# Performance work log

Measured on AMD Instinct MI355X. Metric: run time of the kernel, lower is better.

The kernel has to match this reference:

```python
import jax, jax.numpy as jnp
import numpy as np

B, S, D = 4, 2048, 1024
NH = 16
H2 = NH // 2
F = D // NH  # per-head hidden = 64
EXP = 4
DECAY_CONST = S // 512  # 4
EPS = 1e-5


def setup_inputs() -> dict:
    key = jax.random.key(0)
    ks = jax.random.split(key, 8)
    inp = {
        "x": jax.random.normal(ks[0], (B, S, D), dtype=jnp.float32),
        # token_norm / channel_norm params (LayerNorm init: ones/zeros)
        "g1": jnp.ones((D,), jnp.float32), "b1": jnp.zeros((D,), jnp.float32),
        "g2": jnp.ones((D,), jnp.float32), "b2": jnp.zeros((D,), jnp.float32),
        # per-head input projections [NH, D, F] and output projection
        "Wp": jax.random.normal(ks[1], (NH, D, F), jnp.float32) * 0.02,
        "bp": jnp.zeros((NH, F), jnp.float32),
        "Wo": jax.random.normal(ks[2], (D, D), jnp.float32) * 0.02,
        "bo": jnp.zeros((D,), jnp.float32),
        # ColRepeatCausalLinear: weight = 0.4, bias = 3 ; RowRepeat: -0.3, 0.2
        "w_col": jnp.full((H2, S), 0.4, jnp.float32),
        "b_col": jnp.full((H2, S), 3.0, jnp.float32),
        "w_row": jnp.full((H2, S), -0.3, jnp.float32),
        "b_row": jnp.full((H2, S), 0.2, jnp.float32),
        # decay_value params (ones, clipped to [0.9, 1] then ** (1/decay_constant))
        "dcol": jnp.ones((H2,), jnp.float32),
        "drow": jnp.ones((H2,), jnp.float32),
        # channel MLP
        "W1": jax.random.normal(ks[3], (D, EXP * D), jnp.float32) * 0.02,
        "c1": jnp.zeros((EXP * D,), jnp.float32),
        "W2": jax.random.normal(ks[4], (EXP * D, D), jnp.float32) * 0.02,
        "c2": jnp.zeros((D,), jnp.float32),
    }
    return inp


def _ln(x, g, b):
    m = jnp.mean(x, axis=-1, keepdims=True)
    v = jnp.mean(jnp.square(x - m), axis=-1, keepdims=True)
    return (x - m) * jax.lax.rsqrt(v + EPS) * g + b


def _forward(x, g1, b1, g2, b2, Wp, bp, Wo, bo, w_col, b_col, w_row, b_row,
             dcol, drow, W1, c1, W2, c2):
    decay_c = jnp.clip(dcol, 0.9, 1.0) ** (1.0 / DECAY_CONST)  # [H2]
    decay_r = jnp.clip(drow, 0.9, 1.0) ** (1.0 / DECAY_CONST)  # [H2]

    def step(carry, inp):
        cc, rc = carry                      # each [B, H2, F]
        xt, wc, bc, wr, br = inp            # xt [B, D]; wc/bc/wr/br [H2]
        # token mixing branch
        h = _ln(xt, g1, b1)
        proj = jnp.einsum('bd,hdf->bhf', h, Wp) + bp  # [B, NH, F]
        # Col heads: cache = proj + decay*cache ; out = w*cache + b
        cc = proj[:, :H2] + decay_c[None, :, None] * cc
        col_out = wc[None, :, None] * cc + bc[None, :, None]
        # Row heads: cache = w*proj + decay*cache ; out = cache + b
        rc = wr[None, :, None] * proj[:, H2:] + decay_r[None, :, None] * rc
        row_out = rc + br[None, :, None]
        mix = jnp.concatenate([col_out, row_out], axis=1).reshape(xt.shape[0], -1)
        y = xt + mix @ Wo + bo
        # channel MLP branch
        h2 = _ln(y, g2, b2)
        out = y + jax.nn.gelu(h2 @ W1 + c1) @ W2 + c2
        return (cc, rc), out

    init = (jnp.zeros((x.shape[0], H2, F), x.dtype),
            jnp.zeros((x.shape[0], H2, F), x.dtype))
    xs = (jnp.swapaxes(x, 0, 1), w_col.T, b_col.T, w_row.T, b_row.T)
    _, ys = jax.lax.scan(step, init, xs)    # ys [S, B, D]
    return jnp.swapaxes(ys, 0, 1)


def reference(x, g1, b1, g2, b2, Wp, bp, Wo, bo, w_col, b_col, w_row, b_row,
              dcol, drow, W1, c1, W2, c2):
    return _forward(x, g1, b1, g2, b2, Wp, bp, Wo, bo, w_col, b_col,
                    w_row, b_row, dcol, drow, W1, c1, W2, c2)
```

## Files before the change

### kernel.cpp

```cpp
#include <hip/hip_runtime.h>

typedef __attribute__((ext_vector_type(4))) float fx4;
typedef __attribute__((ext_vector_type(8))) short s16x8;
typedef __attribute__((ext_vector_type(2))) unsigned long long u64x2;

#define SEQ   2048
#define DM    1024
#define BSZ   4
#define ROWS  (BSZ*SEQ)
#define CHUNK 64
#define NCH   (SEQ/CHUNK)

__device__ __forceinline__ unsigned short f2bf(float f){
  unsigned u = __builtin_bit_cast(unsigned, f);
  u = u + 0x7FFFu + ((u >> 16) & 1u);
  return (unsigned short)(u >> 16);
}
__device__ __forceinline__ float bf2f(unsigned short u){
  return __builtin_bit_cast(float, ((unsigned)u) << 16);
}

__device__ __forceinline__ unsigned char f2fp8(float x){
  unsigned u = __builtin_bit_cast(unsigned, x);
  unsigned s = (u >> 24) & 0x80u;
  float ax = __builtin_fabsf(x);
  if (ax >= 448.f) return (unsigned char)(s | 0x7Eu);
  if (ax < 0.015625f){
    int m = (int)(ax * 512.f + 0.5f);
    return (unsigned char)(s | (unsigned)m);
  }
  unsigned b = __builtin_bit_cast(unsigned, ax);
  b += 0x0007FFFFu + ((b >> 20) & 1u);
  unsigned e = (b >> 23) - 127u + 7u;
  unsigned m = (b >> 20) & 7u;
  return (unsigned char)(s | (e << 3) | m);
}

__device__ __forceinline__ float gelu_f(float x){
  float u = 0.7978845608028654f * (x + 0.044715f * x*x*x);
  return x / (1.0f + __expf(-2.0f*u));
}

__device__ __forceinline__ void gload_lds16(const void* g, void* l){
  __builtin_amdgcn_global_load_lds(
      (__attribute__((address_space(1))) void*)g,
      (__attribute__((address_space(3))) void*)l, 16, 0, 0);
}

__device__ __forceinline__ fx4 mfma_fp8(unsigned long long a, unsigned long long b, fx4 c){
  return __builtin_amdgcn_mfma_f32_16x16x32_fp8_fp8((long)a, (long)b, c, 0, 0, 0);
}

__global__ __launch_bounds__(256) void transpose_k(const float* __restrict__ in,
    unsigned short* __restrict__ out, int R, int C, long long ibs, long long obs){
  __shared__ float tile[32][33];
  in  += (long long)blockIdx.z * ibs;
  out += (long long)blockIdx.z * obs;
  int c0 = blockIdx.x*32, r0 = blockIdx.y*32;
  int tx = threadIdx.x, ty = threadIdx.y;
  #pragma unroll
  for (int i=0;i<4;i++)
    tile[ty+8*i][tx] = in[(long long)(r0+ty+8*i)*C + c0+tx];
  __syncthreads();
  #pragma unroll
  for (int i=0;i<4;i++)
    out[(long long)(c0+ty+8*i)*R + r0+tx] = f2bf(tile[tx][ty+8*i]);
}

__global__ __launch_bounds__(256) void transpose_f8(const float* __restrict__ in,
    unsigned char* __restrict__ out, int R, int C){
  __shared__ float tile[32][33];
  int c0 = blockIdx.x*32, r0 = blockIdx.y*32;
  int tx = threadIdx.x, ty = threadIdx.y;
  #pragma unroll
  for (int i=0;i<4;i++)
    tile[ty+8*i][tx] = in[(long long)(r0+ty+8*i)*C + c0+tx];
  __syncthreads();
  #pragma unroll
  for (int i=0;i<4;i++)
    out[(long long)(c0+ty+8*i)*R + r0+tx] = f2fp8(tile[tx][ty+8*i] * 64.f);
}

__global__ __launch_bounds__(256) void ln_rows(const float* __restrict__ x,
    const float* __restrict__ g, const float* __restrict__ b,
    unsigned short* __restrict__ out){
  int row = blockIdx.x, t = threadIdx.x;
  const fx4* xr = (const fx4*)(x + (long long)row*DM);
  fx4 v = xr[t];
  float s  = v[0]+v[1]+v[2]+v[3];
  float s2 = v[0]*v[0]+v[1]*v[1]+v[2]*v[2]+v[3]*v[3];
  #pragma unroll
  for (int o=32;o;o>>=1){ s += __shfl_down(s,o); s2 += __shfl_down(s2,o); }
  __shared__ float red[8];
  int lane = t & 63, wid = t >> 6;
  if (lane==0){ red[wid]=s; red[4+wid]=s2; }
  __syncthreads();
  s  = red[0]+red[1]+red[2]+red[3];
  s2 = red[4]+red[5]+red[6]+red[7];
  float m  = s * (1.0f/DM);
  float rs = rsqrtf(s2*(1.0f/DM) - m*m + 1e-5f);
  const fx4 gv = ((const fx4*)g)[t], bv = ((const fx4*)b)[t];
  ushort4 pk;
  pk.x = f2bf((v[0]-m)*rs*gv[0] + bv[0]);
  pk.y = f2bf((v[1]-m)*rs*gv[1] + bv[1]);
  pk.z = f2bf((v[2]-m)*rs*gv[2] + bv[2]);
  pk.w = f2bf((v[3]-m)*rs*gv[3] + bv[3]);
  *(ushort4*)(out + (long long)row*DM + t*4) = pk;
}

__global__ __launch_bounds__(256) void ln_rows_f8(const float* __restrict__ x,
    const float* __restrict__ g, const float* __restrict__ b,
    unsigned char* __restrict__ out){
  int row = blockIdx.x, t = threadIdx.x;
  const fx4* xr = (const fx4*)(x + (long long)row*DM);
  fx4 v = xr[t];
  float s  = v[0]+v[1]+v[2]+v[3];
  float s2 = v[0]*v[0]+v[1]*v[1]+v[2]*v[2]+v[3]*v[3];
  #pragma unroll
  for (int o=32;o;o>>=1){ s += __shfl_down(s,o); s2 += __shfl_down(s2,o); }
  __shared__ float red[8];
  int lane = t & 63, wid = t >> 6;
  if (lane==0){ red[wid]=s; red[4+wid]=s2; }
  __syncthreads();
  s  = red[0]+red[1]+red[2]+red[3];
  s2 = red[4]+red[5]+red[6]+red[7];
  float m  = s * (1.0f/DM);
  float rs = rsqrtf(s2*(1.0f/DM) - m*m + 1e-5f);
  const fx4 gv = ((const fx4*)g)[t], bv = ((const fx4*)b)[t];
  uchar4 pk;
  pk.x = f2fp8((v[0]-m)*rs*gv[0] + bv[0]);
  pk.y = f2fp8((v[1]-m)*rs*gv[1] + bv[1]);
  pk.z = f2fp8((v[2]-m)*rs*gv[2] + bv[2]);
  pk.w = f2fp8((v[3]-m)*rs*gv[3] + bv[3]);
  *(uchar4*)(out + (long long)row*DM + t*4) = pk;
}

__global__ __launch_bounds__(256) void scan_carry(const unsigned short* __restrict__ P,
    const float* __restrict__ w_row, const float* __restrict__ dcol,
    const float* __restrict__ drow, float* __restrict__ carry){
  int g = blockIdx.x*4 + (threadIdx.x>>6);
  int lane = threadIdx.x & 63;
  int chunk = g & (NCH-1); int bh = g >> 5; int h = bh & 15; int b = bh >> 4;
  float draw = (h<8) ? dcol[h] : drow[h-8];
  float d = powf(fminf(fmaxf(draw,0.9f),1.0f), 0.25f);
  float c = 0.f;
  const unsigned short* p = P + ((long long)(b*SEQ + chunk*CHUNK))*DM + h*64 + lane;
  const float* wr = w_row + (h>=8 ? (h-8)*SEQ + chunk*CHUNK : 0);
  #pragma unroll 4
  for (int i=0;i<CHUNK;i++){
    float a = bf2f(p[(long long)i*DM]);
    if (h>=8) a *= wr[i];
    c = fmaf(d, c, a);
  }
  carry[((long long)(bh*64 + lane))*NCH + chunk] = c;
}

__global__ __launch_bounds__(256) void scan_final(const unsigned short* __restrict__ P,
    const float* __restrict__ w_col, const float* __restrict__ b_col,
    const float* __restrict__ w_row, const float* __restrict__ b_row,
    const float* __restrict__ dcol, const float* __restrict__ drow,
    const float* __restrict__ carry, unsigned short* __restrict__ mix){
  int g = blockIdx.x*4 + (threadIdx.x>>6);
  int lane = threadIdx.x & 63;
  int chunk = g & (NCH-1); int bh = g >> 5; int h = bh & 15; int b = bh >> 4;
  float draw = (h<8) ? dcol[h] : drow[h-8];
  float d = powf(fminf(fmaxf(draw,0.9f),1.0f), 0.25f);
  float dL = d;
  #pragma unroll
  for (int i=0;i<6;i++) dL *= dL;
  const float* cr = carry + ((long long)(bh*64 + lane))*NCH;
  float c = 0.f;
  for (int j=0;j<chunk;j++) c = fmaf(dL, c, cr[j]);
  const unsigned short* p = P + ((long long)(b*SEQ + chunk*CHUNK))*DM + h*64 + lane;
  unsigned short* mo = mix + ((long long)(b*SEQ + chunk*CHUNK))*DM + h*64 + lane;
  int t0 = chunk*CHUNK;
  #pragma unroll 4
  for (int i=0;i<CHUNK;i++){
    int t = t0 + i;
    float a = bf2f(p[(long long)i*DM]);
    float o;
    if (h<8){
      c = fmaf(d, c, a);
      o = w_col[h*SEQ + t]*c + b_col[h*SEQ + t];
    } else {
      a *= w_row[(h-8)*SEQ + t];
      c = fmaf(d, c, a);
      o = c + b_row[(h-8)*SEQ + t];
    }
    mo[(long long)i*DM] = f2bf(o);
  }
}

template<int EPI, int K>
__global__ __launch_bounds__(256) void gemm_bt(const unsigned short* __restrict__ A,
    const unsigned short* __restrict__ Bt, int N,
    const float* __restrict__ bias, const float* __restrict__ res,
    float* __restrict__ outf, unsigned short* __restrict__ outb){
  __shared__ __align__(16) unsigned short lds[16384];
  const int tid = threadIdx.x;
  const int l = tid & 63;
  const int w = tid >> 6;
  const int wr = w >> 1, wc = w & 1;
  const long long row0 = (long long)blockIdx.x * 128;
  const long long col0 = (long long)blockIdx.y * 128;

  fx4 acc[4][4] = {};

  const unsigned short* gA[4];
  const unsigned short* gB[4];
  int lslot[4];
  #pragma unroll
  for (int i=0;i<4;i++){
    int slot = w*256 + i*64 + l;
    int r = slot >> 3;
    int qs = slot & 7;
    int c = (qs ^ (r & 7)) << 3;
    gA[i] = A  + (row0 + r)*(long long)K + c;
    gB[i] = Bt + (col0 + r)*(long long)K + c;
    lslot[i] = slot*8;
  }
  int aoff[2][4], boff[2][4];
  #pragma unroll
  for (int kk=0;kk<2;kk++){
    #pragma unroll
    for (int m=0;m<4;m++){
      int r  = wr*64 + m*16 + (l&15);
      int q  = (kk*4 + (l>>4)) ^ (r&7);
      aoff[kk][m] = r*64 + q*8;
      int r2 = wc*64 + m*16 + (l&15);
      int q2 = (kk*4 + (l>>4)) ^ (r2&7);
      boff[kk][m] = 8192 + r2*64 + q2*8;
    }
  }

  const int nsteps = K >> 6;
  for (int s = 0; s < nsteps; ++s){
    #pragma unroll
    for (int i=0;i<4;i++){
      gload_lds16(gA[i], &lds[lslot[i]]);
      gload_lds16(gB[i], &lds[8192 + lslot[i]]);
      gA[i] += 64; gB[i] += 64;
    }
    __syncthreads();
    #pragma unroll
    for (int kk=0;kk<2;kk++){
      s16x8 af[4], bfr[4];
      #pragma unroll
      for (int m=0;m<4;m++) af[m]  = *(const s16x8*)&lds[aoff[kk][m]];
      #pragma unroll
      for (int n=0;n<4;n++) bfr[n] = *(const s16x8*)&lds[boff[kk][n]];
      #pragma unroll
      for (int m=0;m<4;m++)
        #pragma unroll
        for (int n=0;n<4;n++)
          acc[m][n] = __builtin_amdgcn_mfma_f32_16x16x32_bf16(af[m], bfr[n], acc[m][n], 0, 0, 0);
    }
    __syncthreads();
  }

  float* lf = (float*)lds;
  const int lg = l >> 4, lc = l & 15;
  #pragma unroll
  for (int g=0; g<4; ++g){
    if (wr == (g>>1)){
      #pragma unroll
      for (int mm=0; mm<2; ++mm){
        const int m = (g&1)*2 + mm;
        int lrow = mm*16 + lg*4;
        #pragma unroll
        for (int n=0;n<4;n++){
          int col = wc*64 + n*16 + lc;
          #pragma unroll
          for (int rg=0;rg<4;rg++)
            lf[(lrow+rg)*132 + col] = acc[m][n][rg];
        }
      }
    }
    __syncthreads();
    #pragma unroll
    for (int j=0;j<4;j++){
      int flat = j*256 + tid;
      int lrow = flat >> 5, c4 = flat & 31;
      long long grow = row0 + g*32 + lrow;
      long long gcol = col0 + c4*4;
      fx4 v = *(fx4*)&lf[lrow*132 + c4*4];
      fx4 bv = *(const fx4*)&bias[gcol];
      v = v + bv;
      long long idx = grow*(long long)N + gcol;
      if constexpr (EPI==1){
        fx4 rv = *(const fx4*)&res[idx];
        v = v + rv;
        *(fx4*)&outf[idx] = v;
      } else {
        ushort4 pk;
        pk.x = f2bf(v[0]); pk.y = f2bf(v[1]);
        pk.z = f2bf(v[2]); pk.w = f2bf(v[3]);
        *(ushort4*)&outb[idx] = pk;
      }
    }
    __syncthreads();
  }
}

template<int EPI, int K>
__global__ __launch_bounds__(256) void gemm_f8(const unsigned char* __restrict__ A,
    const unsigned char* __restrict__ Bt, int N,
    const float* __restrict__ bias, const float* __restrict__ res,
    float* __restrict__ outf, unsigned char* __restrict__ outb){
  __shared__ __align__(16) unsigned char lds[49152];
  const int tid = threadIdx.x;
  const int l = tid & 63;
  const int w = tid >> 6;
  const int wr = w >> 1, wc = w & 1;
  const long long row0 = (long long)blockIdx.x * 128;
  const long long col0 = (long long)blockIdx.y * 128;

  fx4 acc[4][4] = {};

  const unsigned char* gA[2];
  const unsigned char* gB[2];
  int lslot[2];
  #pragma unroll
  for (int i=0;i<2;i++){
    int slot = w*128 + i*64 + l;
    int r = slot >> 2;
    int q = slot & 3;
    int c = (q ^ ((r >> 1) & 3)) << 4;
    gA[i] = A  + (row0 + r)*(long long)K + c;
    gB[i] = Bt + (col0 + r)*(long long)K + c;
    lslot[i] = slot*16;
  }
  const int lg = l >> 4, l15 = l & 15;
  int aoff[4], boff[4];
  #pragma unroll
  for (int m=0;m<4;m++){
    int r  = wr*64 + m*16 + l15;
    aoff[m] = r*64 + ((lg ^ ((r >> 1) & 3)) << 4);
    int r2 = wc*64 + m*16 + l15;
    boff[m] = 8192 + r2*64 + ((lg ^ ((r2 >> 1) & 3)) << 4);
  }
  auto STAGE = [&](int bufoff){
    #pragma unroll
    for (int i=0;i<2;i++){
      gload_lds16(gA[i], &lds[bufoff + lslot[i]]);
      gload_lds16(gB[i], &lds[bufoff + 8192 + lslot[i]]);
      gA[i] += 64; gB[i] += 64;
    }
  };

  const int nsteps = K >> 6;
  STAGE(0);
  STAGE(16384);

  int curoff = 0;
  for (int s = 0; s < nsteps; ++s){
    if (s + 1 < nsteps) asm volatile("s_waitcnt vmcnt(4)" ::: "memory");
    else                asm volatile("s_waitcnt vmcnt(0)" ::: "memory");
    __builtin_amdgcn_sched_barrier(0);
    __builtin_amdgcn_s_barrier();
    __builtin_amdgcn_sched_barrier(0);
    u64x2 a2[4], b2[4];
    #pragma unroll
    for (int m=0;m<4;m++) a2[m] = *(const u64x2*)&lds[curoff + aoff[m]];
    #pragma unroll
    for (int n=0;n<4;n++) b2[n] = *(const u64x2*)&lds[curoff + boff[n]];
    if (s + 2 < nsteps){
      int nb = curoff + 32768; if (nb >= 49152) nb -= 49152;
      STAGE(nb);
    }
    #pragma unroll
    for (int m=0;m<4;m++)
      #pragma unroll
      for (int n=0;n<4;n++)
        acc[m][n] = mfma_fp8(a2[m][0], b2[n][0], acc[m][n]);
    #pragma unroll
    for (int m=0;m<4;m++)
      #pragma unroll
      for (int n=0;n<4;n++)
        acc[m][n] = mfma_fp8(a2[m][1], b2[n][1], acc[m][n]);
    curoff += 16384; if (curoff == 49152) curoff = 0;
  }
  __syncthreads();

  float* lf = (float*)lds;
  #pragma unroll
  for (int g=0; g<4; ++g){
    if (wr == (g>>1)){
      #pragma unroll
      for (int mm=0; mm<2; ++mm){
        const int m = (g&1)*2 + mm;
        int lrow = mm*16 + lg*4;
        #pragma unroll
        for (int n=0;n<4;n++){
          int col = wc*64 + n*16 + l15;
          #pragma unroll
          for (int rg=0;rg<4;rg++)
            lf[(lrow+rg)*132 + col] = acc[m][n][rg];
        }
      }
    }
    __syncthreads();
    #pragma unroll
    for (int j=0;j<4;j++){
      int flat = j*256 + tid;
      int lrow = flat >> 5, c4 = flat & 31;
      long long grow = row0 + g*32 + lrow;
      long long gcol = col0 + c4*4;
      fx4 v = *(fx4*)&lf[lrow*132 + c4*4];
      fx4 bv2 = *(const fx4*)&bias[gcol];
      v = v * 0.015625f + bv2;
      long long idx = grow*(long long)N + gcol;
      if constexpr (EPI==1){
        fx4 rv = *(const fx4*)&res[idx];
        v = v + rv;
        *(fx4*)&outf[idx] = v;
      } else {
        uchar4 pk;
        pk.x = f2fp8(gelu_f(v[0]));
        pk.y = f2fp8(gelu_f(v[1]));
        pk.z = f2fp8(gelu_f(v[2]));
        pk.w = f2fp8(gelu_f(v[3]));
        *(uchar4*)&outb[idx] = pk;
      }
    }
    __syncthreads();
  }
}

extern "C" void kernel_launch(void* const* d_in, const int* in_sizes, int n_in,
                              void* d_out, int out_size, void* d_ws, size_t ws_size,
                              hipStream_t stream){
  const float* x    = (const float*)d_in[0];
  const float* g1   = (const float*)d_in[1];
  const float* b1   = (const float*)d_in[2];
  const float* g2   = (const float*)d_in[3];
  const float* b2   = (const float*)d_in[4];
  const float* Wp   = (const float*)d_in[5];
  const float* bp   = (const float*)d_in[6];
  const float* Wo   = (const float*)d_in[7];
  const float* bo   = (const float*)d_in[8];
  const float* w_col= (const float*)d_in[9];
  const float* b_col= (const float*)d_in[10];
  const float* w_row= (const float*)d_in[11];
  const float* b_row= (const float*)d_in[12];
  const float* dcol = (const float*)d_in[13];
  const float* drow = (const float*)d_in[14];
  const float* W1   = (const float*)d_in[15];
  const float* c1   = (const float*)d_in[16];
  const float* W2   = (const float*)d_in[17];
  const float* c2   = (const float*)d_in[18];
  float* out = (float*)d_out;

  char* ws = (char*)d_ws;
  const size_t MB = 1024*1024;
  if (ws_size < 101*MB) return;
  unsigned short* Wpt  = (unsigned short*)(ws + 0);
  unsigned short* Wot  = (unsigned short*)(ws + 2*MB);
  unsigned char*  W1t8 = (unsigned char*)(ws + 4*MB);
  unsigned char*  W2t8 = (unsigned char*)(ws + 12*MB);
  unsigned short* h    = (unsigned short*)(ws + 20*MB);
  unsigned char*  yln8 = (unsigned char*)(ws + 20*MB);
  unsigned short* P    = (unsigned short*)(ws + 36*MB);
  unsigned char*  U8   = (unsigned char*)(ws + 36*MB);
  unsigned short* mix  = (unsigned short*)(ws + 68*MB);
  float*          carry= (float*)(ws + 84*MB);

  dim3 tb(32,8);
  transpose_k <<<dim3(2,32,16),  tb, 0, stream>>>(Wp, Wpt, 1024,   64, 65536LL, 65536LL);
  transpose_k <<<dim3(32,32,1),  tb, 0, stream>>>(Wo, Wot, 1024, 1024, 0LL, 0LL);
  transpose_f8<<<dim3(128,32,1), tb, 0, stream>>>(W1, W1t8, 1024, 4096);
  transpose_f8<<<dim3(32,128,1), tb, 0, stream>>>(W2, W2t8, 4096, 1024);

  ln_rows<<<dim3(ROWS), dim3(256), 0, stream>>>(x, g1, b1, h);
  gemm_bt<3,1024><<<dim3(64,8),  dim3(256), 0, stream>>>(h,   Wpt, 1024, bp, nullptr, nullptr, P);
  scan_carry<<<dim3(512), dim3(256), 0, stream>>>(P, w_row, dcol, drow, carry);
  scan_final<<<dim3(512), dim3(256), 0, stream>>>(P, w_col, b_col, w_row, b_row, dcol, drow, carry, mix);
  gemm_bt<1,1024><<<dim3(64,8),  dim3(256), 0, stream>>>(mix, Wot, 1024, bo, x, out, nullptr);
  ln_rows_f8<<<dim3(ROWS), dim3(256), 0, stream>>>(out, g2, b2, yln8);
  gemm_f8<2,1024><<<dim3(64,32), dim3(256), 0, stream>>>(yln8, W1t8, 4096, c1, nullptr, nullptr, U8);
  gemm_f8<1,4096><<<dim3(64,8),  dim3(256), 0, stream>>>(U8,  W2t8, 1024, c2, out, out, nullptr);
}
```

Before: 281.5 us.

## Triple-buffer bf16 GEMM LDS loads and use hardware fp8 pack conversion

```diff
diff --git a/kernel.cpp b/kernel.cpp
--- a/kernel.cpp
+++ b/kernel.cpp
@@ -34,6 +34,11 @@
   unsigned e = (b >> 23) - 127u + 7u;
   unsigned m = (b >> 20) & 7u;
   return (unsigned char)(s | (e << 3) | m);
+}
+
+__device__ __forceinline__ int pk4_fp8(float a, float b, float c, float d){
+  int lo = __builtin_amdgcn_cvt_pk_fp8_f32(a, b, 0, false);
+  return  __builtin_amdgcn_cvt_pk_fp8_f32(c, d, lo, true);
 }
 
 __device__ __forceinline__ float gelu_f(float x){
@@ -127,12 +132,9 @@
   float m  = s * (1.0f/DM);
   float rs = rsqrtf(s2*(1.0f/DM) - m*m + 1e-5f);
   const fx4 gv = ((const fx4*)g)[t], bv = ((const fx4*)b)[t];
-  uchar4 pk;
-  pk.x = f2fp8((v[0]-m)*rs*gv[0] + bv[0]);
-  pk.y = f2fp8((v[1]-m)*rs*gv[1] + bv[1]);
-  pk.z = f2fp8((v[2]-m)*rs*gv[2] + bv[2]);
-  pk.w = f2fp8((v[3]-m)*rs*gv[3] + bv[3]);
-  *(uchar4*)(out + (long long)row*DM + t*4) = pk;
+  int pk = pk4_fp8((v[0]-m)*rs*gv[0] + bv[0], (v[1]-m)*rs*gv[1] + bv[1],
+                   (v[2]-m)*rs*gv[2] + bv[2], (v[3]-m)*rs*gv[3] + bv[3]);
+  *(int*)(out + (long long)row*DM + t*4) = pk;
 }
 
 __global__ __launch_bounds__(256) void scan_carry(const unsigned short* __restrict__ P,
@@ -196,7 +198,7 @@
     const unsigned short* __restrict__ Bt, int N,
     const float* __restrict__ bias, const float* __restrict__ res,
     float* __restrict__ outf, unsigned short* __restrict__ outb){
-  __shared__ __align__(16) unsigned short lds[16384];
+  __shared__ __align__(16) unsigned short lds[24576];
   const int tid = threadIdx.x;
   const int l = tid & 63;
   const int w = tid >> 6;
@@ -206,60 +208,67 @@
 
   fx4 acc[4][4] = {};
 
-  const unsigned short* gA[4];
-  const unsigned short* gB[4];
-  int lslot[4];
-  #pragma unroll
-  for (int i=0;i<4;i++){
-    int slot = w*256 + i*64 + l;
-    int r = slot >> 3;
-    int qs = slot & 7;
-    int c = (qs ^ (r & 7)) << 3;
+  const unsigned short* gA[2];
+  const unsigned short* gB[2];
+  int lslot[2];
+  #pragma unroll
+  for (int i=0;i<2;i++){
+    int slot = w*128 + i*64 + l;
+    int r = slot >> 2;
+    int q = slot & 3;
+    int c = (q ^ ((r >> 1) & 3)) << 3;
     gA[i] = A  + (row0 + r)*(long long)K + c;
     gB[i] = Bt + (col0 + r)*(long long)K + c;
     lslot[i] = slot*8;
   }
-  int aoff[2][4], boff[2][4];
-  #pragma unroll
-  for (int kk=0;kk<2;kk++){
-    #pragma unroll
-    for (int m=0;m<4;m++){
-      int r  = wr*64 + m*16 + (l&15);
-      int q  = (kk*4 + (l>>4)) ^ (r&7);
-      aoff[kk][m] = r*64 + q*8;
-      int r2 = wc*64 + m*16 + (l&15);
-      int q2 = (kk*4 + (l>>4)) ^ (r2&7);
-      boff[kk][m] = 8192 + r2*64 + q2*8;
-    }
-  }
-
-  const int nsteps = K >> 6;
+  const int lg = l >> 4, l15 = l & 15;
+  int aoff[4], boff[4];
+  #pragma unroll
+  for (int m=0;m<4;m++){
+    int r  = wr*64 + m*16 + l15;
+    aoff[m] = r*32 + ((lg ^ ((r >> 1) & 3)) << 3);
+    int r2 = wc*64 + m*16 + l15;
+    boff[m] = 4096 + r2*32 + ((lg ^ ((r2 >> 1) & 3)) << 3);
+  }
+  auto STAGE = [&](int bufoff){
+    #pragma unroll
+    for (int i=0;i<2;i++){
+      gload_lds16(gA[i], &lds[bufoff + lslot[i]]);
+      gload_lds16(gB[i], &lds[bufoff + 4096 + lslot[i]]);
+      gA[i] += 32; gB[i] += 32;
+    }
+  };
+
+  const int nsteps = K >> 5;
+  STAGE(0);
+  STAGE(8192);
+
+  int curoff = 0;
   for (int s = 0; s < nsteps; ++s){
-    #pragma unroll
-    for (int i=0;i<4;i++){
-      gload_lds16(gA[i], &lds[lslot[i]]);
-      gload_lds16(gB[i], &lds[8192 + lslot[i]]);
-      gA[i] += 64; gB[i] += 64;
-    }
-    __syncthreads();
-    #pragma unroll
-    for (int kk=0;kk<2;kk++){
-      s16x8 af[4], bfr[4];
+    if (s + 1 < nsteps) asm volatile("s_waitcnt vmcnt(4)" ::: "memory");
+    else                asm volatile("s_waitcnt vmcnt(0)" ::: "memory");
+    __builtin_amdgcn_sched_barrier(0);
+    __builtin_amdgcn_s_barrier();
+    __builtin_amdgcn_sched_barrier(0);
+    s16x8 af[4], bfr[4];
+    #pragma unroll
+    for (int m=0;m<4;m++) af[m]  = *(const s16x8*)&lds[curoff + aoff[m]];
+    #pragma unroll
+    for (int n=0;n<4;n++) bfr[n] = *(const s16x8*)&lds[curoff + boff[n]];
+    if (s + 2 < nsteps){
+      int nb = curoff + 16384; if (nb >= 24576) nb -= 24576;
+      STAGE(nb);
+    }
+    #pragma unroll
+    for (int m=0;m<4;m++)
       #pragma unroll
-      for (int m=0;m<4;m++) af[m]  = *(const s16x8*)&lds[aoff[kk][m]];
-      #pragma unroll
-      for (int n=0;n<4;n++) bfr[n] = *(const s16x8*)&lds[boff[kk][n]];
-      #pragma unroll
-      for (int m=0;m<4;m++)
-        #pragma unroll
-        for (int n=0;n<4;n++)
-          acc[m][n] = __builtin_amdgcn_mfma_f32_16x16x32_bf16(af[m], bfr[n], acc[m][n], 0, 0, 0);
-    }
-    __syncthreads();
-  }
+      for (int n=0;n<4;n++)
+        acc[m][n] = __builtin_amdgcn_mfma_f32_16x16x32_bf16(af[m], bfr[n], acc[m][n], 0, 0, 0);
+    curoff += 8192; if (curoff == 24576) curoff = 0;
+  }
+  __syncthreads();
 
   float* lf = (float*)lds;
-  const int lg = l >> 4, lc = l & 15;
   #pragma unroll
   for (int g=0; g<4; ++g){
     if (wr == (g>>1)){
@@ -269,7 +278,7 @@
         int lrow = mm*16 + lg*4;
         #pragma unroll
         for (int n=0;n<4;n++){
-          int col = wc*64 + n*16 + lc;
+          int col = wc*64 + n*16 + l15;
           #pragma unroll
           for (int rg=0;rg<4;rg++)
             lf[(lrow+rg)*132 + col] = acc[m][n][rg];
@@ -415,12 +424,8 @@
         v = v + rv;
         *(fx4*)&outf[idx] = v;
       } else {
-        uchar4 pk;
-        pk.x = f2fp8(gelu_f(v[0]));
-        pk.y = f2fp8(gelu_f(v[1]));
-        pk.z = f2fp8(gelu_f(v[2]));
-        pk.w = f2fp8(gelu_f(v[3]));
-        *(uchar4*)&outb[idx] = pk;
+        *(int*)&outb[idx] = pk4_fp8(gelu_f(v[0]), gelu_f(v[1]),
+                                    gelu_f(v[2]), gelu_f(v[3]));
       }
     }
     __syncthreads();
```

After: 271.7 us. 3.5% less time.

## Widen FP8 GEMM tile to 128x256 and use hardware FP8 pack conversion

Applied to the files above, without the earlier changes.

```diff
diff --git a/kernel.cpp b/kernel.cpp
--- a/kernel.cpp
+++ b/kernel.cpp
@@ -34,6 +34,11 @@
   unsigned e = (b >> 23) - 127u + 7u;
   unsigned m = (b >> 20) & 7u;
   return (unsigned char)(s | (e << 3) | m);
+}
+
+__device__ __forceinline__ int pk4_fp8(float a, float b, float c, float d){
+  int lo = __builtin_amdgcn_cvt_pk_fp8_f32(a, b, 0, false);
+  return  __builtin_amdgcn_cvt_pk_fp8_f32(c, d, lo, true);
 }
 
 __device__ __forceinline__ float gelu_f(float x){
@@ -127,12 +132,9 @@
   float m  = s * (1.0f/DM);
   float rs = rsqrtf(s2*(1.0f/DM) - m*m + 1e-5f);
   const fx4 gv = ((const fx4*)g)[t], bv = ((const fx4*)b)[t];
-  uchar4 pk;
-  pk.x = f2fp8((v[0]-m)*rs*gv[0] + bv[0]);
-  pk.y = f2fp8((v[1]-m)*rs*gv[1] + bv[1]);
-  pk.z = f2fp8((v[2]-m)*rs*gv[2] + bv[2]);
-  pk.w = f2fp8((v[3]-m)*rs*gv[3] + bv[3]);
-  *(uchar4*)(out + (long long)row*DM + t*4) = pk;
+  int pk = pk4_fp8((v[0]-m)*rs*gv[0] + bv[0], (v[1]-m)*rs*gv[1] + bv[1],
+                   (v[2]-m)*rs*gv[2] + bv[2], (v[3]-m)*rs*gv[3] + bv[3]);
+  *(int*)(out + (long long)row*DM + t*4) = pk;
 }
 
 __global__ __launch_bounds__(256) void scan_carry(const unsigned short* __restrict__ P,
@@ -307,106 +309,119 @@
     const unsigned char* __restrict__ Bt, int N,
     const float* __restrict__ bias, const float* __restrict__ res,
     float* __restrict__ outf, unsigned char* __restrict__ outb){
-  __shared__ __align__(16) unsigned char lds[49152];
+  __shared__ __align__(16) unsigned char lds[73728];
   const int tid = threadIdx.x;
   const int l = tid & 63;
-  const int w = tid >> 6;
-  const int wr = w >> 1, wc = w & 1;
+  const int wcn = tid >> 6;
   const long long row0 = (long long)blockIdx.x * 128;
-  const long long col0 = (long long)blockIdx.y * 128;
-
-  fx4 acc[4][4] = {};
+  const long long col0 = (long long)blockIdx.y * 256;
+
+  fx4 acc[8][4] = {};
 
   const unsigned char* gA[2];
-  const unsigned char* gB[2];
-  int lslot[2];
+  int lslotA[2];
   #pragma unroll
   for (int i=0;i<2;i++){
-    int slot = w*128 + i*64 + l;
+    int slot = wcn*128 + i*64 + l;
     int r = slot >> 2;
     int q = slot & 3;
     int c = (q ^ ((r >> 1) & 3)) << 4;
-    gA[i] = A  + (row0 + r)*(long long)K + c;
+    gA[i] = A + (row0 + r)*(long long)K + c;
+    lslotA[i] = slot*16;
+  }
+  const unsigned char* gB[4];
+  int lslotB[4];
+  #pragma unroll
+  for (int i=0;i<4;i++){
+    int slot = wcn*256 + i*64 + l;
+    int r = slot >> 2;
+    int q = slot & 3;
+    int c = (q ^ ((r >> 1) & 3)) << 4;
     gB[i] = Bt + (col0 + r)*(long long)K + c;
-    lslot[i] = slot*16;
+    lslotB[i] = 8192 + slot*16;
   }
   const int lg = l >> 4, l15 = l & 15;
-  int aoff[4], boff[4];
-  #pragma unroll
-  for (int m=0;m<4;m++){
-    int r  = wr*64 + m*16 + l15;
+  int aoff[8], boff[4];
+  #pragma unroll
+  for (int m=0;m<8;m++){
+    int r = m*16 + l15;
     aoff[m] = r*64 + ((lg ^ ((r >> 1) & 3)) << 4);
-    int r2 = wc*64 + m*16 + l15;
-    boff[m] = 8192 + r2*64 + ((lg ^ ((r2 >> 1) & 3)) << 4);
+  }
+  #pragma unroll
+  for (int n=0;n<4;n++){
+    int r2 = wcn*64 + n*16 + l15;
+    boff[n] = 8192 + r2*64 + ((lg ^ ((r2 >> 1) & 3)) << 4);
   }
   auto STAGE = [&](int bufoff){
     #pragma unroll
     for (int i=0;i<2;i++){
-      gload_lds16(gA[i], &lds[bufoff + lslot[i]]);
-      gload_lds16(gB[i], &lds[bufoff + 8192 + lslot[i]]);
-      gA[i] += 64; gB[i] += 64;
+      gload_lds16(gA[i], &lds[bufoff + lslotA[i]]);
+      gA[i] += 64;
+    }
+    #pragma unroll
+    for (int i=0;i<4;i++){
+      gload_lds16(gB[i], &lds[bufoff + lslotB[i]]);
+      gB[i] += 64;
     }
   };
 
   const int nsteps = K >> 6;
   STAGE(0);
-  STAGE(16384);
+  STAGE(24576);
 
   int curoff = 0;
   for (int s = 0; s < nsteps; ++s){
-    if (s + 1 < nsteps) asm volatile("s_waitcnt vmcnt(4)" ::: "memory");
+    if (s + 1 < nsteps) asm volatile("s_waitcnt vmcnt(6)" ::: "memory");
     else                asm volatile("s_waitcnt vmcnt(0)" ::: "memory");
     __builtin_amdgcn_sched_barrier(0);
     __builtin_amdgcn_s_barrier();
     __builtin_amdgcn_sched_barrier(0);
-    u64x2 a2[4], b2[4];
-    #pragma unroll
-    for (int m=0;m<4;m++) a2[m] = *(const u64x2*)&lds[curoff + aoff[m]];
+    u64x2 a2[8], b2[4];
+    #pragma unroll
+    for (int m=0;m<8;m++) a2[m] = *(const u64x2*)&lds[curoff + aoff[m]];
     #pragma unroll
     for (int n=0;n<4;n++) b2[n] = *(const u64x2*)&lds[curoff + boff[n]];
     if (s + 2 < nsteps){
-      int nb = curoff + 32768; if (nb >= 49152) nb -= 49152;
+      int nb = curoff + 49152; if (nb >= 73728) nb -= 73728;
       STAGE(nb);
     }
     #pragma unroll
-    for (int m=0;m<4;m++)
+    for (int m=0;m<8;m++)
       #pragma unroll
       for (int n=0;n<4;n++)
         acc[m][n] = mfma_fp8(a2[m][0], b2[n][0], acc[m][n]);
     #pragma unroll
-    for (int m=0;m<4;m++)
+    for (int m=0;m<8;m++)
       #pragma unroll
       for (int n=0;n<4;n++)
         acc[m][n] = mfma_fp8(a2[m][1], b2[n][1], acc[m][n]);
-    curoff += 16384; if (curoff == 49152) curoff = 0;
+    curoff += 24576; if (curoff == 73728) curoff = 0;
   }
   __syncthreads();
 
   float* lf = (float*)lds;
   #pragma unroll
   for (int g=0; g<4; ++g){
-    if (wr == (g>>1)){
-      #pragma unroll
-      for (int mm=0; mm<2; ++mm){
-        const int m = (g&1)*2 + mm;
-        int lrow = mm*16 + lg*4;
+    #pragma unroll
+    for (int mm=0; mm<2; ++mm){
+      const int m = g*2 + mm;
+      int lrow = mm*16 + lg*4;
+      #pragma unroll
+      for (int n=0;n<4;n++){
+        int col = wcn*64 + n*16 + l15;
         #pragma unroll
-        for (int n=0;n<4;n++){
-          int col = wc*64 + n*16 + l15;
-          #pragma unroll
-          for (int rg=0;rg<4;rg++)
-            lf[(lrow+rg)*132 + col] = acc[m][n][rg];
-        }
+        for (int rg=0;rg<4;rg++)
+          lf[(lrow+rg)*260 + col] = acc[m][n][rg];
       }
     }
     __syncthreads();
     #pragma unroll
-    for (int j=0;j<4;j++){
+    for (int j=0;j<8;j++){
       int flat = j*256 + tid;
-      int lrow = flat >> 5, c4 = flat & 31;
+      int lrow = flat >> 6, c4 = flat & 63;
       long long grow = row0 + g*32 + lrow;
       long long gcol = col0 + c4*4;
-      fx4 v = *(fx4*)&lf[lrow*132 + c4*4];
+      fx4 v = *(fx4*)&lf[lrow*260 + c4*4];
       fx4 bv2 = *(const fx4*)&bias[gcol];
       v = v * 0.015625f + bv2;
       long long idx = grow*(long long)N + gcol;
@@ -415,12 +430,8 @@
         v = v + rv;
         *(fx4*)&outf[idx] = v;
       } else {
-        uchar4 pk;
-        pk.x = f2fp8(gelu_f(v[0]));
-        pk.y = f2fp8(gelu_f(v[1]));
-        pk.z = f2fp8(gelu_f(v[2]));
-        pk.w = f2fp8(gelu_f(v[3]));
-        *(uchar4*)&outb[idx] = pk;
+        *(int*)&outb[idx] = pk4_fp8(gelu_f(v[0]), gelu_f(v[1]),
+                                    gelu_f(v[2]), gelu_f(v[3]));
       }
     }
     __syncthreads();
@@ -477,6 +488,6 @@
   scan_final<<<dim3(512), dim3(256), 0, stream>>>(P, w_col, b_col, w_row, b_row, dcol, drow, carry, mix);
   gemm_bt<1,1024><<<dim3(64,8),  dim3(256), 0, stream>>>(mix, Wot, 1024, bo, x, out, nullptr);
   ln_rows_f8<<<dim3(ROWS), dim3(256), 0, stream>>>(out, g2, b2, yln8);
-  gemm_f8<2,1024><<<dim3(64,32), dim3(256), 0, stream>>>(yln8, W1t8, 4096, c1, nullptr, nullptr, U8);
-  gemm_f8<1,4096><<<dim3(64,8),  dim3(256), 0, stream>>>(U8,  W2t8, 1024, c2, out, out, nullptr);
-}
+  gemm_f8<2,1024><<<dim3(64,16), dim3(256), 0, stream>>>(yln8, W1t8, 4096, c1, nullptr, nullptr, U8);
+  gemm_f8<1,4096><<<dim3(64,4),  dim3(256), 0, stream>>>(U8,  W2t8, 1024, c2, out, out, nullptr);
+}
```

Measured after the change: 329.2 us. +16.9%, slower.
